# Kernel tuning notes

Measured on AMD Instinct MI355X. Metric: run time of the kernel, lower is better.

## Reference

```python
import jax, jax.numpy as jnp
import numpy as np
from jax import lax

B, T, D = 4, 4096, 1024  # d_inner == D (expansion=1.0)


def setup_inputs() -> dict:
    key = jax.random.key(0)
    ks = jax.random.split(key, 6)
    s = 1.0 / np.sqrt(D)  # xavier-ish scale
    return {
        "x": jax.random.normal(ks[0], (B, T, D), dtype=jnp.float32),
        "W_in": jax.random.normal(ks[1], (D, D), dtype=jnp.float32) * s,
        "W_alpha": jax.random.normal(ks[2], (D, D), dtype=jnp.float32) * s,
        "b_alpha": jnp.full((D,), 2.0, dtype=jnp.float32),
        "W_beta": jax.random.normal(ks[3], (D, D), dtype=jnp.float32) * s,
        "b_beta": jnp.zeros((D,), dtype=jnp.float32),
        "W_v": jax.random.normal(ks[4], (D, D), dtype=jnp.float32) * s,
        "b_v": jnp.zeros((D,), dtype=jnp.float32),
        "W_out": jax.random.normal(ks[5], (D, D), dtype=jnp.float32) * s,
    }


def reference(x, W_in, W_alpha, b_alpha, W_beta, b_beta, W_v, b_v, W_out):
    # x: [B, T, D]; torch nn.Linear convention y = x @ W.T
    xp = jax.nn.silu(jnp.einsum("btd,ed->bte", x, W_in))  # [B, T, Di]
    alpha = jax.nn.sigmoid(jnp.einsum("bte,fe->btf", xp, W_alpha) + b_alpha)
    beta = jax.nn.sigmoid(jnp.einsum("bte,fe->btf", xp, W_beta) + b_beta)
    v = jnp.tanh(jnp.einsum("bte,fe->btf", xp, W_v) + b_v)
    bv = beta * v  # precompute write term

    def step(h, ab):
        a_t, bv_t = ab  # each [B, Di]
        h = a_t * h + bv_t
        return h, h * jax.nn.silu(h)

    h0 = jnp.zeros((x.shape[0], W_alpha.shape[0]), dtype=x.dtype)
    h_last, outs = lax.scan(step, h0, (alpha.transpose(1, 0, 2), bv.transpose(1, 0, 2)))
    cell_out = outs.transpose(1, 0, 2)  # [B, T, Di]
    output = jnp.einsum("btf,df->btd", cell_out, W_out)
    return output, h_last
```

## Files before the change

kernel.cpp:

```cpp
#include <hip/hip_runtime.h>
#include <hip/hip_bf16.h>
#include <cstdint>
#include <cstddef>

typedef __bf16 bf16_t;
typedef _Float16 f16_t;
typedef __bf16 bf16x2 __attribute__((ext_vector_type(2)));
typedef __bf16 bf16x4 __attribute__((ext_vector_type(4)));
typedef __bf16 bf16x8 __attribute__((ext_vector_type(8)));
typedef _Float16 f16x2 __attribute__((ext_vector_type(2)));
typedef float  f32x16 __attribute__((ext_vector_type(16)));

constexpr int kBatch = 4;
constexpr int kT = 4096;
constexpr int kD = 1024;
constexpr int kM = kBatch * kT;
constexpr int kCH = kBatch * kD;
constexpr int kNC = 128;
constexpr int kL  = kT / kNC;
constexpr int LDS_BYTES = 65536;

__device__ __forceinline__ size_t tiled_idx(int r, int c, int ktiles) {
    return (size_t)((r >> 7) * ktiles + (c >> 6)) * 8192
         + (((r >> 5) & 3) << 11) + (((c >> 4) & 3) << 9)
         + (((c >> 3) & 1) << 8) + ((r & 31) << 3) + (c & 7);
}

__device__ __forceinline__ void async16(const bf16_t* g, char* l) {
    __builtin_amdgcn_global_load_lds(
        (const __attribute__((address_space(1))) uint32_t*)g,
        (__attribute__((address_space(3))) uint32_t*)l,
        16, 0, 0);
}

__device__ __forceinline__ float fast_sigmoid(float z) {
    return 1.f / (1.f + __expf(-z));
}
__device__ __forceinline__ float fast_tanh(float z) {
    z = fminf(10.f, fmaxf(-10.f, z));
    float e = __expf(2.f * z);
    return (e - 1.f) / (e + 1.f);
}

__global__ __launch_bounds__(256)
void cvt_all_kernel(const float* __restrict__ x,
                    const float* __restrict__ w0, const float* __restrict__ w1,
                    const float* __restrict__ w2, const float* __restrict__ w3,
                    const float* __restrict__ w4,
                    bf16_t* __restrict__ xd, bf16_t* __restrict__ wd)
{
    __shared__ __align__(16) bf16_t sl[8192];
    int tile = blockIdx.x;
    const float* src; bf16_t* dst; int loc;
    if (tile < 2048) { src = x; dst = xd; loc = tile; }
    else {
        int seg = (tile - 2048) >> 7;
        loc = (tile - 2048) & 127;
        src = seg == 0 ? w0 : seg == 1 ? w1 : seg == 2 ? w2 : seg == 3 ? w3 : w4;
        dst = wd + (size_t)seg * kD * kD;
    }
    const int rt = loc >> 4, kt = loc & 15;
    const int tid = threadIdx.x;
    const int c4 = tid & 15;
    const int rl0 = tid >> 4;
    const int coff = (((c4 >> 2) & 3) << 9) + (((c4 >> 1) & 1) << 8) + ((c4 & 1) << 2);
#pragma unroll
    for (int p = 0; p < 8; ++p) {
        const int r = p * 16 + rl0;
        float4 a = reinterpret_cast<const float4*>(src)[(size_t)(rt * 128 + r) * 256 + kt * 16 + c4];
        bf16x4 o;
        o[0] = (bf16_t)a.x; o[1] = (bf16_t)a.y; o[2] = (bf16_t)a.z; o[3] = (bf16_t)a.w;
        *reinterpret_cast<bf16x4*>(&sl[((r >> 5) << 11) + ((r & 31) << 3) + coff]) = o;
    }
    __syncthreads();
    bf16x8* d8 = reinterpret_cast<bf16x8*>(dst) + (size_t)loc * 1024;
    const bf16x8* s8 = reinterpret_cast<const bf16x8*>(sl);
#pragma unroll
    for (int j = 0; j < 4; ++j)
        d8[tid + j * 256] = s8[tid + j * 256];
}

template<int EPI>
__global__ __launch_bounds__(256, 2)
void gemm128(const bf16_t* __restrict__ A, const bf16_t* __restrict__ Bw,
             const float* __restrict__ bi0, const float* __restrict__ bi1,
             const float* __restrict__ bi2,
             void* __restrict__ out0, void* __restrict__ out1, void* __restrict__ out2,
             int M, int N, int K)
{
    extern __shared__ char lds[];
    const int tid  = threadIdx.x;
    const int lane = tid & 63;
    const int wv   = tid >> 6;
    const int wr   = wv >> 1;
    const int wc   = wv & 1;
    const int l32  = lane & 31;
    const int lh   = lane >> 5;

    int bid = blockIdx.y * gridDim.x + blockIdx.x;
    int nwg = gridDim.x * gridDim.y;
    int swz = (bid & 7) * (nwg >> 3) + (bid >> 3);
    int gx  = N >> 7;
    int n0  = (swz % gx) << 7;
    int m0  = (swz / gx) << 7;

    const int ktiles = K >> 6;
    const size_t arow = (size_t)(m0 >> 7) * ktiles * 8192;
    const size_t brow = (size_t)(n0 >> 7) * ktiles * 8192;
    const int tid16 = tid << 4;

    auto STAGE_TILE = [&](int w, int bufo) {
        const bf16_t* at = A + arow + (size_t)w * 8192;
        const bf16_t* bt = Bw + brow + (size_t)w * 8192;
#pragma unroll
        for (int j = 0; j < 4; ++j) {
            async16(at + ((size_t)(j * 256 + tid)) * 8, lds + bufo + j * 4096 + tid16);
            async16(bt + ((size_t)(j * 256 + tid)) * 8, lds + bufo + 16384 + j * 4096 + tid16);
        }
    };

    const int lane16 = lane << 4;
    int offA[2][4], offB[2][4];
#pragma unroll
    for (int mi = 0; mi < 2; ++mi)
#pragma unroll
        for (int ks = 0; ks < 4; ++ks) {
            offA[mi][ks] = ((wr * 2 + mi) << 12) + (ks << 10) + lane16;
            offB[mi][ks] = 16384 + ((wc * 2 + mi) << 12) + (ks << 10) + lane16;
        }

    f32x16 acc[2][2];
#pragma unroll
    for (int i = 0; i < 2; ++i)
#pragma unroll
        for (int j = 0; j < 2; ++j)
            acc[i][j] = (f32x16)(0.f);

    const int NT = K >> 6;

    STAGE_TILE(0, 0);
    asm volatile("s_waitcnt vmcnt(0)" ::: "memory");
    asm volatile("s_barrier" ::: "memory");

    for (int w = 0; w < NT; ++w) {
        const int bufo  = (w & 1) << 15;
        const int nbufo = bufo ^ 32768;

        if (w + 1 < NT) STAGE_TILE(w + 1, nbufo);

#pragma unroll
        for (int ks = 0; ks < 4; ++ks) {
            bf16x8 aF[2], bF[2];
#pragma unroll
            for (int mi = 0; mi < 2; ++mi) {
                aF[mi] = *reinterpret_cast<const bf16x8*>(lds + bufo + offA[mi][ks]);
                bF[mi] = *reinterpret_cast<const bf16x8*>(lds + bufo + offB[mi][ks]);
            }
            __builtin_amdgcn_s_setprio(1);
#pragma unroll
            for (int mi = 0; mi < 2; ++mi)
#pragma unroll
                for (int ni = 0; ni < 2; ++ni)
                    acc[mi][ni] = __builtin_amdgcn_mfma_f32_32x32x16_bf16(aF[mi], bF[ni], acc[mi][ni], 0, 0, 0);
            __builtin_amdgcn_s_setprio(0);
        }

        if (w + 1 < NT) {
            asm volatile("s_waitcnt vmcnt(0)" ::: "memory");
            asm volatile("s_barrier" ::: "memory");
        }
    }

    const int slab = n0 >> 10;
    const float* bia = (EPI == 4) ? (slab == 0 ? bi0 : slab == 1 ? bi1 : bi2) : nullptr;
#pragma unroll
    for (int nf = 0; nf < 2; ++nf) {
        const int colg = n0 + wc * 64 + nf * 32 + l32;
        const int cL = colg & (kD - 1);
        float bs = 0.f;
        if constexpr (EPI == 4) bs = bia[cL];
#pragma unroll
        for (int mf = 0; mf < 2; ++mf) {
            const int rbase = m0 + wr * 64 + mf * 32 + lh * 4;
#pragma unroll
            for (int rg = 0; rg < 16; ++rg) {
                const int rowg = rbase + (rg & 3) + ((rg >> 2) << 3);
                const float f = acc[mf][nf][rg];
                if constexpr (EPI == 0) {
                    float s = f * fast_sigmoid(f);
                    reinterpret_cast<bf16_t*>(out0)[tiled_idx(rowg, colg, N >> 6)] = (bf16_t)s;
                } else if constexpr (EPI == 3) {
                    __builtin_nontemporal_store(f, reinterpret_cast<float*>(out0) + (size_t)rowg * N + colg);
                } else {
                    const size_t idx = (size_t)rowg * kD + cL;
                    if (slab == 0) {
                        reinterpret_cast<f16_t*>(out0)[idx] = (f16_t)fast_sigmoid(f + bs);
                    } else if (slab == 1) {
                        reinterpret_cast<bf16_t*>(out1)[idx] = (bf16_t)fast_sigmoid(f + bs);
                    } else {
                        reinterpret_cast<bf16_t*>(out2)[idx] = (bf16_t)fast_tanh(f + bs);
                    }
                }
            }
        }
    }
}

__global__ void scan_chunk_kernel(const f16_t* __restrict__ alpha,
                                  const bf16_t* __restrict__ beta,
                                  const bf16_t* __restrict__ vv,
                                  float* __restrict__ Aagg,
                                  float* __restrict__ Bagg)
{
    const int u2  = blockIdx.x * blockDim.x + threadIdx.x;
    const int ch2 = u2 & 2047;
    const int c   = u2 >> 11;
    const int b   = ch2 >> 9;
    const int d   = (ch2 & 511) << 1;
    size_t base = ((size_t)b * kT + (size_t)c * kL) * kD + d;
    float A0 = 1.f, B0 = 0.f, A1 = 1.f, B1 = 0.f;
#pragma unroll 4
    for (int t = 0; t < kL; ++t) {
        f16x2  a2 = *reinterpret_cast<const f16x2*>(alpha + base);
        bf16x2 b2 = *reinterpret_cast<const bf16x2*>(beta + base);
        bf16x2 v2 = *reinterpret_cast<const bf16x2*>(vv + base);
        float bv0 = (float)b2[0] * (float)v2[0];
        float bv1 = (float)b2[1] * (float)v2[1];
        A0 *= (float)a2[0]; B0 = (float)a2[0] * B0 + bv0;
        A1 *= (float)a2[1]; B1 = (float)a2[1] * B1 + bv1;
        base += kD;
    }
    const size_t o = (size_t)c * kCH + 2 * ch2;
    *reinterpret_cast<float2*>(Aagg + o) = make_float2(A0, A1);
    *reinterpret_cast<float2*>(Bagg + o) = make_float2(B0, B1);
}

__global__ void scan_mid_kernel(const float* __restrict__ Aagg,
                                const float* __restrict__ Bagg,
                                float* __restrict__ Hin,
                                float* __restrict__ hlast)
{
    const int ch = blockIdx.x * blockDim.x + threadIdx.x;
    float h = 0.f;
#pragma unroll 8
    for (int c = 0; c < kNC; ++c) {
        Hin[(size_t)c * kCH + ch] = h;
        h = Aagg[(size_t)c * kCH + ch] * h + Bagg[(size_t)c * kCH + ch];
    }
    hlast[ch] = h;
}

__global__ void scan_out_kernel(const f16_t* __restrict__ alpha,
                                const bf16_t* __restrict__ beta,
                                const bf16_t* __restrict__ vv,
                                const float* __restrict__ Hin,
                                bf16_t* __restrict__ cell)
{
    const int u2  = blockIdx.x * blockDim.x + threadIdx.x;
    const int ch2 = u2 & 2047;
    const int c   = u2 >> 11;
    const int b   = ch2 >> 9;
    const int d   = (ch2 & 511) << 1;
    size_t base = ((size_t)b * kT + (size_t)c * kL) * kD + d;
    const size_t tb = (size_t)((b * 32 + (c >> 2)) * 16 + (d >> 6)) * 8192
                    + ((size_t)(c & 3) << 11) + (((d >> 4) & 3) << 9)
                    + (((d >> 3) & 1) << 8) + (d & 7);
    float2 h2 = *reinterpret_cast<const float2*>(Hin + (size_t)c * kCH + 2 * ch2);
    float h0 = h2.x, h1 = h2.y;
#pragma unroll 4
    for (int t = 0; t < kL; ++t) {
        f16x2  a2 = *reinterpret_cast<const f16x2*>(alpha + base);
        bf16x2 b2 = *reinterpret_cast<const bf16x2*>(beta + base);
        bf16x2 v2 = *reinterpret_cast<const bf16x2*>(vv + base);
        h0 = (float)a2[0] * h0 + (float)b2[0] * (float)v2[0];
        h1 = (float)a2[1] * h1 + (float)b2[1] * (float)v2[1];
        bf16x2 o;
        o[0] = (bf16_t)(h0 * h0 * fast_sigmoid(h0));
        o[1] = (bf16_t)(h1 * h1 * fast_sigmoid(h1));
        *reinterpret_cast<bf16x2*>(cell + tb + t * 8) = o;
        base += kD;
    }
}

extern "C" void kernel_launch(void* const* d_in, const int* in_sizes, int n_in,
                              void* d_out, int out_size, void* d_ws, size_t ws_size,
                              hipStream_t stream)
{
    const float* x     = (const float*)d_in[0];
    const float* W_in  = (const float*)d_in[1];
    const float* W_al  = (const float*)d_in[2];
    const float* b_al  = (const float*)d_in[3];
    const float* W_be  = (const float*)d_in[4];
    const float* b_be  = (const float*)d_in[5];
    const float* W_v   = (const float*)d_in[6];
    const float* b_v   = (const float*)d_in[7];
    const float* W_out = (const float*)d_in[8];

    float* out   = (float*)d_out;
    float* hlast = out + (size_t)kM * kD;

    char* ws = (char*)d_ws;
    size_t off = 0;
    auto alloc = [&](size_t bytes) -> void* {
        void* p = ws + off;
        off += (bytes + 255) & ~(size_t)255;
        return p;
    };
    bf16_t* xbf   = (bf16_t*)alloc((size_t)kM * kD * 2);
    bf16_t* xp    = (bf16_t*)alloc((size_t)kM * kD * 2);
    f16_t*  alpha = (f16_t*) alloc((size_t)kM * kD * 2);
    bf16_t* betab = (bf16_t*)alloc((size_t)kM * kD * 2);
    bf16_t* vb    = (bf16_t*)alloc((size_t)kM * kD * 2);
    bf16_t* wbf   = (bf16_t*)alloc((size_t)5 * kD * kD * 2);

    bf16_t* Winb = wbf;
    bf16_t* Wfus = wbf + 1 * (size_t)kD * kD;
    bf16_t* Wob  = wbf + 4 * (size_t)kD * kD;

    bf16_t* cell = xbf;
    float*  Aagg = (float*)xp;
    float*  Bagg = Aagg + (size_t)kNC * kCH;
    float*  Hin  = Bagg + (size_t)kNC * kCH;

    hipFuncSetAttribute(reinterpret_cast<const void*>(gemm128<0>), hipFuncAttributeMaxDynamicSharedMemorySize, LDS_BYTES);
    hipFuncSetAttribute(reinterpret_cast<const void*>(gemm128<3>), hipFuncAttributeMaxDynamicSharedMemorySize, LDS_BYTES);
    hipFuncSetAttribute(reinterpret_cast<const void*>(gemm128<4>), hipFuncAttributeMaxDynamicSharedMemorySize, LDS_BYTES);

    cvt_all_kernel<<<2048 + 5 * 128, 256, 0, stream>>>(x, W_in, W_al, W_be, W_v, W_out,
                                                       xbf, wbf);

    dim3 grid1(kD / 128, kM / 128);
    dim3 gridF(3 * kD / 128, kM / 128);

    gemm128<0><<<grid1, 256, LDS_BYTES, stream>>>(xbf, Winb, nullptr, nullptr, nullptr,
                                                  xp, nullptr, nullptr, kM, kD, kD);
    gemm128<4><<<gridF, 256, LDS_BYTES, stream>>>(xp, Wfus, b_al, b_be, b_v,
                                                  alpha, betab, vb, kM, 3 * kD, kD);
    scan_chunk_kernel<<<kNC * kCH / 512, 256, 0, stream>>>(alpha, betab, vb, Aagg, Bagg);
    scan_mid_kernel<<<kCH / 256, 256, 0, stream>>>(Aagg, Bagg, Hin, hlast);
    scan_out_kernel<<<kNC * kCH / 512, 256, 0, stream>>>(alpha, betab, vb, Hin, cell);

    gemm128<3><<<grid1, 256, LDS_BYTES, stream>>>(cell, Wob, nullptr, nullptr, nullptr,
                                                  out, nullptr, nullptr, kM, kD, kD);
}
```

Before: 320.1 us.

## Load GEMM B fragments directly from global into registers, halve LDS

The B operand tiles are no longer staged through LDS. Each wave loads its B fragments straight from global memory into registers with inline global_load_dwordx4, so LDS holds only double-buffered A tiles. LDS drops to 32KB and launch bounds rise to 3 blocks per CU to improve occupancy. The trade-off is that B rows are reloaded per wave instead of shared across waves through LDS, which raises global/L2 traffic, and the hand-counted vmcnt waits make correctness depend on instruction ordering.

```diff
diff --git a/kernel.cpp b/kernel.cpp
--- a/kernel.cpp
+++ b/kernel.cpp
@@ -18,7 +18,7 @@
 constexpr int kCH = kBatch * kD;
 constexpr int kNC = 128;
 constexpr int kL  = kT / kNC;
-constexpr int LDS_BYTES = 65536;
+constexpr int LDS_BYTES = 32768;
 
 __device__ __forceinline__ size_t tiled_idx(int r, int c, int ktiles) {
     return (size_t)((r >> 7) * ktiles + (c >> 6)) * 8192
@@ -81,7 +81,7 @@
 }
 
 template<int EPI>
-__global__ __launch_bounds__(256, 2)
+__global__ __launch_bounds__(256, 3)
 void gemm128(const bf16_t* __restrict__ A, const bf16_t* __restrict__ Bw,
              const float* __restrict__ bi0, const float* __restrict__ bi1,
              const float* __restrict__ bi2,
@@ -109,25 +109,22 @@
     const size_t brow = (size_t)(n0 >> 7) * ktiles * 8192;
     const int tid16 = tid << 4;
 
-    auto STAGE_TILE = [&](int w, int bufo) {
+    auto STAGE_A = [&](int w, int bufo) {
         const bf16_t* at = A + arow + (size_t)w * 8192;
-        const bf16_t* bt = Bw + brow + (size_t)w * 8192;
-#pragma unroll
-        for (int j = 0; j < 4; ++j) {
+#pragma unroll
+        for (int j = 0; j < 4; ++j)
             async16(at + ((size_t)(j * 256 + tid)) * 8, lds + bufo + j * 4096 + tid16);
-            async16(bt + ((size_t)(j * 256 + tid)) * 8, lds + bufo + 16384 + j * 4096 + tid16);
-        }
     };
 
+    const bf16_t* bwave = Bw + brow + ((size_t)(wc << 1) << 11) + (size_t)lane * 8;
+
     const int lane16 = lane << 4;
-    int offA[2][4], offB[2][4];
+    int offA[2][4];
 #pragma unroll
     for (int mi = 0; mi < 2; ++mi)
 #pragma unroll
-        for (int ks = 0; ks < 4; ++ks) {
+        for (int ks = 0; ks < 4; ++ks)
             offA[mi][ks] = ((wr * 2 + mi) << 12) + (ks << 10) + lane16;
-            offB[mi][ks] = 16384 + ((wc * 2 + mi) << 12) + (ks << 10) + lane16;
-        }
 
     f32x16 acc[2][2];
 #pragma unroll
@@ -138,32 +135,47 @@
 
     const int NT = K >> 6;
 
-    STAGE_TILE(0, 0);
+    STAGE_A(0, 0);
     asm volatile("s_waitcnt vmcnt(0)" ::: "memory");
     asm volatile("s_barrier" ::: "memory");
 
     for (int w = 0; w < NT; ++w) {
-        const int bufo  = (w & 1) << 15;
-        const int nbufo = bufo ^ 32768;
-
-        if (w + 1 < NT) STAGE_TILE(w + 1, nbufo);
-
-#pragma unroll
-        for (int ks = 0; ks < 4; ++ks) {
-            bf16x8 aF[2], bF[2];
-#pragma unroll
-            for (int mi = 0; mi < 2; ++mi) {
-                aF[mi] = *reinterpret_cast<const bf16x8*>(lds + bufo + offA[mi][ks]);
-                bF[mi] = *reinterpret_cast<const bf16x8*>(lds + bufo + offB[mi][ks]);
-            }
-            __builtin_amdgcn_s_setprio(1);
+        const int bufo  = (w & 1) << 14;
+        const int nbufo = bufo ^ 16384;
+
+        bf16x8 bF[2][4];
+        const bf16_t* bt = bwave + (size_t)w * 8192;
+#pragma unroll
+        for (int nb = 0; nb < 2; ++nb)
+#pragma unroll
+            for (int ks = 0; ks < 4; ++ks)
+                asm volatile("global_load_dwordx4 %0, %1, off"
+                             : "=v"(bF[nb][ks])
+                             : "v"(bt + (size_t)nb * 2048 + ks * 512)
+                             : "memory");
+
+        if (w + 1 < NT) STAGE_A(w + 1, nbufo);
+
+        bf16x8 aF[2][4];
+#pragma unroll
+        for (int mi = 0; mi < 2; ++mi)
+#pragma unroll
+            for (int ks = 0; ks < 4; ++ks)
+                aF[mi][ks] = *reinterpret_cast<const bf16x8*>(lds + bufo + offA[mi][ks]);
+
+        if (w + 1 < NT) { asm volatile("s_waitcnt vmcnt(4)" ::: "memory"); }
+        else           { asm volatile("s_waitcnt vmcnt(0)" ::: "memory"); }
+        __builtin_amdgcn_sched_barrier(0);
+
+        __builtin_amdgcn_s_setprio(1);
+#pragma unroll
+        for (int ks = 0; ks < 4; ++ks)
 #pragma unroll
             for (int mi = 0; mi < 2; ++mi)
 #pragma unroll
                 for (int ni = 0; ni < 2; ++ni)
-                    acc[mi][ni] = __builtin_amdgcn_mfma_f32_32x32x16_bf16(aF[mi], bF[ni], acc[mi][ni], 0, 0, 0);
-            __builtin_amdgcn_s_setprio(0);
-        }
+                    acc[mi][ni] = __builtin_amdgcn_mfma_f32_32x32x16_bf16(aF[mi][ks], bF[ni][ks], acc[mi][ni], 0, 0, 0);
+        __builtin_amdgcn_s_setprio(0);
 
         if (w + 1 < NT) {
             asm volatile("s_waitcnt vmcnt(0)" ::: "memory");
```

Result: slower. 337.4 us (+5.4%).
